# Optimization experiments

Hardware: AMD Instinct MI355X
Metric: run time of the kernel (lower is better)

## Reference

```python
import math
import jax, jax.numpy as jnp
import numpy as np

H = 768      # hidden_size
NH = 12      # num_attention_heads
K = 3        # attention_num branches (wid = None, 2, 4)
DIV = 5.0    # gauss_divisor = 2**(attention_num-1) + 1
SFT = 1.0    # sft_factor
WIDTHS = (None, 2.0, 4.0)
B, L = 4, 1024


def _layernorm(x, s, b, eps=1e-5):
    m = jnp.mean(x, axis=-1, keepdims=True)
    v = jnp.mean((x - m) ** 2, axis=-1, keepdims=True)
    return (x - m) / jnp.sqrt(v + eps) * s + b


def _log_gauss_bias(props_len, width):
    # matches generate_gauss_weight + log(clamp_min(1e-6))
    center = jnp.arange(props_len, dtype=jnp.float32) / props_len          # (L,)
    wt = jnp.maximum(jnp.float32(width), 0.01) / DIV                       # scalar
    pos = jnp.linspace(0.0, 1.0, props_len)                                # (L,)
    g = (0.3989422804014327 / wt) * jnp.exp(-(pos[None, :] - center[:, None]) ** 2 / (2.0 * wt * wt))
    g = g / jnp.max(g, axis=-1, keepdims=True)
    return jnp.log(jnp.maximum(g, 1e-6))                                   # (L, L)


def _attn(qx, kx, vx, Wq, bq, Wk, bk, Wv, bv, bias, mask):
    Bn, Lq, D = qx.shape
    dh = D // NH
    q = (qx @ Wq + bq).reshape(Bn, Lq, NH, dh)
    k = (kx @ Wk + bk).reshape(Bn, kx.shape[1], NH, dh)
    v = (vx @ Wv + bv).reshape(Bn, vx.shape[1], NH, dh)
    s = jnp.einsum('bqhd,bkhd->bhqk', q, k) / math.sqrt(dh)
    if bias is not None:
        s = s + bias[None, None]                  # cached Gaussian log-bias
    if mask is not None:
        s = s + (1.0 - mask)[:, None, None, :] * (-10000.0)
    p = jax.nn.softmax(s, axis=-1)
    return jnp.einsum('bhqk,bkhd->bqhd', p, v).reshape(Bn, Lq, D)


def _block(x, mask, Wq, bq, Wk, bk, Wv, bv, W1, b1, W2, b2, n1s, n1b, n2s, n2b, bias):
    a = _attn(x, x, x, Wq, bq, Wk, bk, Wv, bv, bias, mask)
    x = _layernorm(x + a, n1s, n1b)
    h = jax.nn.relu(x @ W1 + b1) @ W2 + b2
    return _layernorm(x + h, n2s, n2b)


def setup_inputs():
    key = jax.random.key(0)
    ks = iter(jax.random.split(key, 64))
    def p(*sh):
        return jax.random.normal(next(ks), sh, dtype=jnp.float32) * 0.02
    inp = {}
    inp['input_tensor'] = jax.random.normal(next(ks), (B, L, H), dtype=jnp.float32)
    inp['attention_mask'] = jnp.ones((B, L), dtype=jnp.float32)
    for nm, sh in [('bWq', (K, H, H)), ('bWk', (K, H, H)), ('bWv', (K, H, H)),
                   ('bW1', (K, H, 4 * H)), ('bW2', (K, 4 * H, H)),
                   ('caWq', (H, H)), ('caWk', (H, H)), ('caWv', (H, H)),
                   ('caW1', (H, H)), ('caW2', (H, H)), ('Wl1', (H, H)), ('Wl2', (H, 1))]:
        inp[nm] = p(*sh)
    for nm, sh in [('bbq', (K, H)), ('bbk', (K, H)), ('bbv', (K, H)), ('bb1', (K, 4 * H)), ('bb2', (K, H)),
                   ('cabq', (H,)), ('cabk', (H,)), ('cabv', (H,)), ('cab1', (H,)), ('cab2', (H,)),
                   ('bl1', (H,)), ('bl2', (1,))]:
        inp[nm] = jnp.zeros(sh, dtype=jnp.float32)
    for nm, sh in [('bn1s', (K, H)), ('bn2s', (K, H)), ('bns', (H,)), ('can1s', (H,)), ('can2s', (H,))]:
        inp[nm] = jnp.ones(sh, dtype=jnp.float32)
    for nm, sh in [('bn1b', (K, H)), ('bn2b', (K, H)), ('bnb', (H,)), ('can1b', (H,)), ('can2b', (H,))]:
        inp[nm] = jnp.zeros(sh, dtype=jnp.float32)
    return inp


def reference(input_tensor, attention_mask, bWq, bbq, bWk, bbk, bWv, bbv, bW1, bb1, bW2, bb2,
              bn1s, bn1b, bn2s, bn2b, bns, bnb,
              caWq, cabq, caWk, cabk, caWv, cabv, caW1, cab1, caW2, cab2,
              can1s, can1b, can2s, can2b, Wl1, bl1, Wl2, bl2):
    Bn, Ln, _ = input_tensor.shape
    mask = attention_mask
    biases = [None if w is None else _log_gauss_bias(Ln, w) for w in WIDTHS]
    outs = []
    for i in range(K):
        o = _block(input_tensor, mask,
                   bWq[i], bbq[i], bWk[i], bbk[i], bWv[i], bbv[i],
                   bW1[i], bb1[i], bW2[i], bb2[i],
                   bn1s[i], bn1b[i], bn2s[i], bn2b[i], biases[i])
        outs.append(_layernorm(o, bns, bnb))
    oo = jnp.stack(outs, axis=-1)                                   # (B, L, H, K)
    valid = mask                                                    # (B, L)
    denom = jnp.maximum(valid.sum(axis=1, keepdims=True), 1.0)      # (B, 1)
    mean_token = (oo.mean(-1) * valid[:, :, None]).sum(axis=1, keepdims=True) / denom[:, :, None]  # (B,1,H)
    selected = mean_token  # weight_token=None, mode='global' -> global_token = mean_token
    branch_feat = jnp.transpose(oo, (0, 3, 1, 2)).reshape(Bn * K, Ln, H)
    query_token = jnp.repeat(selected, K, axis=0)                   # (B*K, 1, H)
    branch_mask = jnp.repeat(mask, K, axis=0)                       # (B*K, L)
    # CrossAttention (wid=None, FFN d_ff = H)
    a = _attn(query_token, branch_feat, branch_feat, caWq, cabq, caWk, cabk, caWv, cabv, None, branch_mask)
    q = _layernorm(query_token + a, can1s, can1b)
    t = jax.nn.relu(q @ caW1 + cab1) @ caW2 + cab2
    q = _layernorm(q + t, can2s, can2b)                             # (B*K, 1, H)
    w = q.reshape(Bn, K, H)
    w = jax.nn.relu(w @ Wl1 + bl1)
    w = (w @ Wl2 + bl2)[..., 0]                                     # (B, K)
    w = jax.nn.softmax(w / SFT, axis=-1)
    return (oo * w[:, None, None, :]).sum(axis=-1)                  # (B, L, H)
```

## Files before the change

### kernel.cpp

```cpp
#include <hip/hip_runtime.h>
#include <hip/hip_bf16.h>
#include <cstdint>
#include <cmath>

typedef __hip_bfloat16 bf16;
typedef __attribute__((ext_vector_type(8))) __bf16 bf16x8;
typedef __attribute__((ext_vector_type(4))) float f32x4;

#define NE2C ((size_t)4096 * 768)

__device__ inline float ldv(const void* __restrict__ p, size_t i, bool b){
  return b ? __bfloat162float(((const bf16*)p)[i]) : ((const float*)p)[i];
}

__device__ inline float wave_sum(float v){
  #pragma unroll
  for (int o = 1; o < 64; o <<= 1) v += __shfl_xor(v, o, 64);
  return v;
}
__device__ inline float wave_max(float v){
  #pragma unroll
  for (int o = 1; o < 64; o <<= 1) v = fmaxf(v, __shfl_xor(v, o, 64));
  return v;
}

__device__ __forceinline__ void gload_lds16(const __bf16* g, __bf16* l){
  __builtin_amdgcn_global_load_lds(
      (const __attribute__((address_space(1))) uint32_t*)g,
      (__attribute__((address_space(3))) uint32_t*)l,
      16, 0, 0);
}

__global__ void flag_kernel(const void* __restrict__ bns, int* __restrict__ flagp){
  if (threadIdx.x == 0) flagp[0] = (((const uint32_t*)bns)[0] == 0x3F800000u) ? 0 : 1;
}

__global__ __launch_bounds__(256) void maskchk_kernel(const void* __restrict__ mask, int* __restrict__ flagp){
  const bool isb = flagp[0] != 0;
  int t = threadIdx.x;
  int ok = 1;
  for (int j = t; j < 4096; j += 256) ok &= (ldv(mask, (size_t)j, isb) == 1.0f) ? 1 : 0;
  __shared__ int allok;
  if (t == 0) allok = 1;
  __syncthreads();
  if (!ok) atomicAnd(&allok, 0);
  __syncthreads();
  if (t == 0) flagp[1] = allok;
}

__global__ __launch_bounds__(256) void cvtb_kernel(const void* __restrict__ in, __bf16* __restrict__ out,
                                                   int n, const int* __restrict__ flagp){
  const bool isb = flagp[0] != 0;
  int i = blockIdx.x * 256 + threadIdx.x;
  if (i < n) out[i] = (__bf16)ldv(in, i, isb);
}

__global__ __launch_bounds__(256) void transpose_kernel(const void* __restrict__ in, size_t in_off, size_t in_zstride,
    __bf16* __restrict__ out, size_t out_off, size_t out_zstride, int K, int N, const int* __restrict__ flagp)
{
  const bool isb = flagp[0] != 0;
  const int z = blockIdx.z;
  const size_t ioff = in_off + (size_t)z * in_zstride;
  __bf16* op = out + out_off + (size_t)z * out_zstride;
  const int n0 = blockIdx.x * 64, k0 = blockIdx.y * 64;
  __shared__ __bf16 T[64][65];
  const int cr = threadIdx.x >> 6, cc = threadIdx.x & 63;
  #pragma unroll
  for (int it = 0; it < 16; ++it) {
    int r = it * 4 + cr;
    T[r][cc] = (__bf16)ldv(in, ioff + (size_t)(k0 + r) * N + (n0 + cc), isb);
  }
  __syncthreads();
  #pragma unroll
  for (int it = 0; it < 16; ++it) {
    int r = it * 4 + cr;
    op[(size_t)(n0 + r) * K + (k0 + cc)] = T[cc][r];
  }
}

__global__ __launch_bounds__(256) void biaspack_kernel(const void* bbq, const void* bbk, const void* bbv,
    const void* bb1, const void* bb2, const void* cabk, const void* cabv,
    float* __restrict__ pool, const int* __restrict__ flagp)
{
  const bool isb = flagp[0] != 0;
  int idx = blockIdx.x * 256 + threadIdx.x;
  if (idx >= 19968) return;
  float v;
  if (idx < 6912) {
    int i = idx / 2304, rem = idx % 2304;
    int m = rem / 768, c = rem % 768;
    const void* src = (m == 0) ? bbq : ((m == 1) ? bbk : bbv);
    v = ldv(src, (size_t)i * 768 + c, isb);
  } else if (idx < 16128) v = ldv(bb1, idx - 6912, isb);
  else if (idx < 18432)   v = ldv(bb2, idx - 16128, isb);
  else if (idx < 19200)   v = ldv(cabk, idx - 18432, isb);
  else                    v = ldv(cabv, idx - 19200, isb);
  pool[idx] = v;
}

__global__ __launch_bounds__(256) void gaussbias_kernel(float* __restrict__ gb)
{
  const int br = blockIdx.x >> 10;
  const int q  = blockIdx.x & 1023;
  const float inv2wt2 = (br == 0) ? 3.125f : 0.78125f;
  const float c2 = inv2wt2 * 1.4426950408889634f;
  const float cq = (float)q * (1.f / 1024.f);
  const float kst = roundf(cq * 1023.f);
  const float dd = kst * (1.f / 1023.f) - cq;
  const float dmin = dd * dd;
  float* row = gb + (size_t)br * 1048576 + (size_t)q * 1024;
  for (int o = threadIdx.x; o < 1024; o += 256) {
    int cb = o >> 6, rem = o & 63, rr = rem >> 2, t = rem & 3;
    int k = cb * 64 + t * 16 + rr;
    float d2 = (float)k * (1.f / 1023.f) - cq;
    row[o] = fmaxf((dmin - d2 * d2) * c2, -19.9315686f);
  }
}

__global__ __launch_bounds__(256) void gemm_mfma_kernel(
    const __bf16* __restrict__ A, size_t a_zstride,
    const __bf16* __restrict__ WT, const float* __restrict__ biasp,
    __bf16* __restrict__ C, int M, int N, int K, int relu)
{
  const int z = blockIdx.z;
  A  += (size_t)z * a_zstride;
  WT += (size_t)z * (size_t)N * K;
  biasp += (size_t)z * N;
  C  += (size_t)z * (size_t)M * N;
  const int m0 = blockIdx.y * 128, n0 = blockIdx.x * 128;
  const int tid = threadIdx.x, w = tid >> 6, lane = tid & 63;
  const int quad = lane >> 4, r16 = lane & 15;
  const int wr = w >> 1, wc = w & 1;
  __shared__ __align__(16) __bf16 As[128 * 32];
  __shared__ __align__(16) __bf16 Bs[128 * 32];
  f32x4 acc[4][4];
  #pragma unroll
  for (int i = 0; i < 4; ++i)
    #pragma unroll
    for (int j = 0; j < 4; ++j) acc[i][j] = (f32x4){0.f, 0.f, 0.f, 0.f};

  const int srow = tid >> 2;
  const int scc  = (tid & 3) * 8;

  for (int k0 = 0; k0 < K; k0 += 32) {
    __syncthreads();
    #pragma unroll
    for (int it = 0; it < 2; ++it) {
      int row = it * 64 + srow;
      const __bf16* gA = A  + (size_t)(m0 + row) * K + k0 + scc;
      const __bf16* gB = WT + (size_t)(n0 + row) * K + k0 + scc;
      __bf16* lA = &As[(it * 256 + w * 64) * 8];
      __bf16* lB = &Bs[(it * 256 + w * 64) * 8];
      gload_lds16(gA, lA);
      gload_lds16(gB, lB);
    }
    __syncthreads();
    bf16x8 af[4], bf[4];
    #pragma unroll
    for (int mt = 0; mt < 4; ++mt) af[mt] = *(const bf16x8*)&As[(wr * 64 + mt * 16 + r16) * 32 + quad * 8];
    #pragma unroll
    for (int nt = 0; nt < 4; ++nt) bf[nt] = *(const bf16x8*)&Bs[(wc * 64 + nt * 16 + r16) * 32 + quad * 8];
    #pragma unroll
    for (int mt = 0; mt < 4; ++mt)
      #pragma unroll
      for (int nt = 0; nt < 4; ++nt)
        acc[mt][nt] = __builtin_amdgcn_mfma_f32_16x16x32_bf16(af[mt], bf[nt], acc[mt][nt], 0, 0, 0);
  }
  #pragma unroll
  for (int nt = 0; nt < 4; ++nt) {
    int col = n0 + wc * 64 + nt * 16 + r16;
    float bv = biasp[col];
    #pragma unroll
    for (int mt = 0; mt < 4; ++mt) {
      int rowb = m0 + wr * 64 + mt * 16 + quad * 4;
      #pragma unroll
      for (int reg = 0; reg < 4; ++reg) {
        float v = acc[mt][nt][reg] + bv;
        if (relu) v = fmaxf(v, 0.f);
        C[(size_t)(rowb + reg) * N + col] = (__bf16)v;
      }
    }
  }
}

__global__ __launch_bounds__(256) void gemm_small_kernel(const float* __restrict__ A, const void* __restrict__ W,
    size_t woff, const void* __restrict__ bias, size_t boff, float* __restrict__ C,
    int N, int K, int relu, const int* __restrict__ flagp)
{
  const bool isb = flagp[0] != 0;
  const int row = blockIdx.y;
  const int c = blockIdx.x * 64 + (threadIdx.x & 63);
  const int ks = threadIdx.x >> 6;
  const int klen = K >> 2;
  const float* ar = A + (size_t)row * K + ks * klen;
  const size_t wbase = woff + (size_t)ks * klen * N + c;
  float acc = 0.f;
  #pragma unroll 4
  for (int k = 0; k < klen; ++k)
    acc += ar[k] * ldv(W, wbase + (size_t)k * N, isb);
  __shared__ float red[4][64];
  red[ks][threadIdx.x & 63] = acc;
  __syncthreads();
  if (threadIdx.x < 64) {
    float v = red[0][threadIdx.x] + red[1][threadIdx.x] + red[2][threadIdx.x] + red[3][threadIdx.x];
    v += ldv(bias, boff + c, isb);
    if (relu) v = fmaxf(v, 0.f);
    C[(size_t)row * N + c] = v;
  }
}

__global__ __launch_bounds__(256) void attn_mfma_kernel(
    const __bf16* __restrict__ QKV, const void* __restrict__ mask,
    const float* __restrict__ gbias,
    __bf16* __restrict__ Aout, const int* __restrict__ flagp)
{
  const bool isb = flagp[0] != 0;
  const bool mall = flagp[1] != 0;
  const int bz = blockIdx.z;
  const int b = bz & 3, br = bz >> 2;
  const __bf16* Q  = QKV + (size_t)br * 3 * NE2C;
  const __bf16* Kg = Q + NE2C;
  const __bf16* Vg = Q + 2 * NE2C;
  Aout += (size_t)br * NE2C;
  const int has_bias = br > 0;

  const int h = blockIdx.y;
  const int tid = threadIdx.x;
  const int w = tid >> 6, lane = tid & 63;
  const int quad = lane >> 4, r16 = lane & 15;
  const int qbase = blockIdx.x * 64 + w * 16;

  __shared__ __align__(16) __bf16 Ks[64 * 72];
  __shared__ __align__(16) __bf16 Vt[64 * 72];
  __shared__ __align__(16) __bf16 Ps[4][16 * 72];

  const __bf16* qrow = Q + ((size_t)(b * 1024 + qbase + r16)) * 768 + h * 64;
  bf16x8 aq0 = *(const bf16x8*)(qrow + quad * 8);
  bf16x8 aq1 = *(const bf16x8*)(qrow + 32 + quad * 8);

  const float* bq4[4];
  if (has_bias) {
    const float* gbb = gbias + (size_t)(br - 1) * 1048576 + r16 * 4;
    #pragma unroll
    for (int reg = 0; reg < 4; ++reg)
      bq4[reg] = gbb + (size_t)(qbase + quad * 4 + reg) * 1024;
  }

  float m_r[4], l_r[4];
  f32x4 O[4];
  #pragma unroll
  for (int n = 0; n < 4; ++n) O[n] = (f32x4){0.f, 0.f, 0.f, 0.f};
  #pragma unroll
  for (int reg = 0; reg < 4; ++reg) { m_r[reg] = -1e30f; l_r[reg] = 0.f; }

  const int dd = tid & 63;
  const int rb = tid >> 6;
  const int dswz = (dd >> 3) & 7;

  const int kr_row0 = tid >> 3;
  const int kr_c8   = (tid & 7) * 8;
  const size_t kcol  = (size_t)h * 64 + kr_c8;
  const size_t vcol  = (size_t)h * 64 + dd;
  const size_t bbase = (size_t)b * 1024;

  const float SCL = 0.18033688f;
  const float MBIG = 14426.9504f;
  const float THR2 = 11.5415603f;

  bf16x8 kpre0, kpre1;
  bf16x8 vpre0, vpre1;

  {
    kpre0 = *(const bf16x8*)(Kg + (bbase + kr_row0)      * 768 + kcol);
    kpre1 = *(const bf16x8*)(Kg + (bbase + kr_row0 + 32) * 768 + kcol);
    const int r0 = rb * 16;
    #pragma unroll
    for (int i = 0; i < 8; ++i) {
      vpre0[i] = Vg[(bbase + r0 + i)     * 768 + vcol];
      vpre1[i] = Vg[(bbase + r0 + 8 + i) * 768 + vcol];
    }
  }

  for (int c0 = 0; c0 < 1024; c0 += 64) {
    __syncthreads();
    *(bf16x8*)&Ks[kr_row0 * 72 + kr_c8]        = kpre0;
    *(bf16x8*)&Ks[(kr_row0 + 32) * 72 + kr_c8] = kpre1;
    {
      int blk0 = ((rb * 16)     >> 3) ^ dswz;
      int blk1 = ((rb * 16 + 8) >> 3) ^ dswz;
      *(bf16x8*)&Vt[dd * 72 + blk0 * 8] = vpre0;
      *(bf16x8*)&Vt[dd * 72 + blk1 * 8] = vpre1;
    }
    __syncthreads();

    if (c0 + 64 < 1024) {
      const size_t cb = bbase + c0 + 64;
      kpre0 = *(const bf16x8*)(Kg + (cb + kr_row0)      * 768 + kcol);
      kpre1 = *(const bf16x8*)(Kg + (cb + kr_row0 + 32) * 768 + kcol);
      const int r0 = rb * 16;
      #pragma unroll
      for (int i = 0; i < 8; ++i) {
        vpre0[i] = Vg[(cb + r0 + i)     * 768 + vcol];
        vpre1[i] = Vg[(cb + r0 + 8 + i) * 768 + vcol];
      }
    }

    f32x4 bv4[4];
    if (has_bias) {
      #pragma unroll
      for (int reg = 0; reg < 4; ++reg) bv4[reg] = *(const f32x4*)(bq4[reg] + c0);
    }

    float s4[4][4], p4[4][4];
    #pragma unroll
    for (int t = 0; t < 4; ++t) {
      bf16x8 b0 = *(const bf16x8*)&Ks[(t * 16 + r16) * 72 + quad * 8];
      bf16x8 b1 = *(const bf16x8*)&Ks[(t * 16 + r16) * 72 + 32 + quad * 8];
      f32x4 accq = (f32x4){0.f, 0.f, 0.f, 0.f};
      accq = __builtin_amdgcn_mfma_f32_16x16x32_bf16(aq0, b0, accq, 0, 0, 0);
      accq = __builtin_amdgcn_mfma_f32_16x16x32_bf16(aq1, b1, accq, 0, 0, 0);
      float mterm = 0.f;
      if (!mall) {
        int kk = c0 + t * 16 + r16;
        float mk = ldv(mask, (size_t)(b * 1024 + kk), isb);
        mterm = fmaf(mk, MBIG, -MBIG);
      }
      if (has_bias) {
        #pragma unroll
        for (int reg = 0; reg < 4; ++reg)
          s4[t][reg] = fmaf(accq[reg], SCL, mterm) + bv4[reg][t];
      } else {
        #pragma unroll
        for (int reg = 0; reg < 4; ++reg)
          s4[t][reg] = fmaf(accq[reg], SCL, mterm);
      }
    }
    float mlane[4];
    #pragma unroll
    for (int reg = 0; reg < 4; ++reg)
      mlane[reg] = fmaxf(fmaxf(s4[0][reg], s4[1][reg]), fmaxf(s4[2][reg], s4[3][reg]));
    bool need = (mlane[0] > m_r[0] + THR2) || (mlane[1] > m_r[1] + THR2)
             || (mlane[2] > m_r[2] + THR2) || (mlane[3] > m_r[3] + THR2);
    if (__any(need)) {
      #pragma unroll
      for (int reg = 0; reg < 4; ++reg) {
        float t0 = mlane[reg];
        #pragma unroll
        for (int off = 1; off < 16; off <<= 1) t0 = fmaxf(t0, __shfl_xor(t0, off, 64));
        float mnew = fmaxf(m_r[reg], t0);
        float alpha = exp2f(m_r[reg] - mnew);
        l_r[reg] *= alpha;
        m_r[reg] = mnew;
        #pragma unroll
        for (int n = 0; n < 4; ++n) O[n][reg] *= alpha;
      }
    }
    #pragma unroll
    for (int reg = 0; reg < 4; ++reg) {
      float rs = 0.f;
      #pragma unroll
      for (int t = 0; t < 4; ++t) { float p = exp2f(s4[t][reg] - m_r[reg]); p4[t][reg] = p; rs += p; }
      l_r[reg] += rs;
    }
    __bf16* pw = &Ps[w][0];
    #pragma unroll
    for (int t = 0; t < 4; ++t)
      #pragma unroll
      for (int reg = 0; reg < 4; ++reg)
        pw[(quad * 4 + reg) * 72 + t * 16 + r16] = (__bf16)p4[t][reg];
    bf16x8 ap0 = *(const bf16x8*)&pw[r16 * 72 + quad * 8];
    bf16x8 ap1 = *(const bf16x8*)&pw[r16 * 72 + 32 + quad * 8];
    __builtin_amdgcn_s_setprio(1);
    #pragma unroll
    for (int n = 0; n < 4; ++n) {
      int dr = n * 16 + r16;
      int sw = (dr >> 3) & 7;
      bf16x8 bv0 = *(const bf16x8*)&Vt[dr * 72 + (quad ^ sw) * 8];
      bf16x8 bv1 = *(const bf16x8*)&Vt[dr * 72 + ((quad + 4) ^ sw) * 8];
      O[n] = __builtin_amdgcn_mfma_f32_16x16x32_bf16(ap0, bv0, O[n], 0, 0, 0);
      O[n] = __builtin_amdgcn_mfma_f32_16x16x32_bf16(ap1, bv1, O[n], 0, 0, 0);
    }
    __builtin_amdgcn_s_setprio(0);
  }
  #pragma unroll
  for (int reg = 0; reg < 4; ++reg) {
    float lv = l_r[reg];
    #pragma unroll
    for (int off = 1; off < 16; off <<= 1) lv += __shfl_xor(lv, off, 64);
    l_r[reg] = lv;
  }
  #pragma unroll
  for (int n = 0; n < 4; ++n)
    #pragma unroll
    for (int reg = 0; reg < 4; ++reg) {
      int qg = qbase + quad * 4 + reg;
      Aout[((size_t)(b * 1024 + qg)) * 768 + h * 64 + n * 16 + r16] = (__bf16)(O[n][reg] / l_r[reg]);
    }
}

__global__ __launch_bounds__(256) void lnb_b_kernel(const __bf16* __restrict__ x, const __bf16* __restrict__ a,
    const void* __restrict__ sc, const void* __restrict__ bi, __bf16* __restrict__ out,
    const int* __restrict__ flagp)
{
  const bool isb = flagp[0] != 0;
  const int br = blockIdx.y;
  a   += (size_t)br * NE2C;
  out += (size_t)br * NE2C;
  const size_t so = (size_t)br * 768;
  int r = blockIdx.x;
  const __bf16* xr = x + (size_t)r * 768;
  const __bf16* ar = a + (size_t)r * 768;
  int t = threadIdx.x;
  float v[3]; float s = 0.f, ss = 0.f;
  #pragma unroll
  for (int j = 0; j < 3; j++) {
    int c = t + j * 256;
    float val = (float)xr[c] + (float)ar[c];
    v[j] = val; s += val; ss += val * val;
  }
  s = wave_sum(s); ss = wave_sum(ss);
  __shared__ float sred[8];
  __shared__ float stats[2];
  int lane = t & 63, wid = t >> 6;
  if (lane == 0) { sred[wid] = s; sred[4 + wid] = ss; }
  __syncthreads();
  if (t == 0) {
    float S = sred[0] + sred[1] + sred[2] + sred[3];
    float SS = sred[4] + sred[5] + sred[6] + sred[7];
    float mean = S * (1.f / 768.f);
    float var = fmaxf(SS * (1.f / 768.f) - mean * mean, 0.f);
    stats[0] = mean; stats[1] = rsqrtf(var + 1e-5f);
  }
  __syncthreads();
  float mean = stats[0], rstd = stats[1];
  #pragma unroll
  for (int j = 0; j < 3; j++) {
    int c = t + j * 256;
    out[(size_t)r * 768 + c] = (__bf16)((v[j] - mean) * rstd * ldv(sc, so + c, isb) + ldv(bi, so + c, isb));
  }
}

__global__ __launch_bounds__(256) void lnb2_b_kernel(const __bf16* __restrict__ x, const __bf16* __restrict__ a,
    const void* __restrict__ sc1, const void* __restrict__ bi1,
    const void* __restrict__ sc2, const void* __restrict__ bi2,
    __bf16* __restrict__ out, const int* __restrict__ flagp)
{
  const bool isb = flagp[0] != 0;
  const int br = blockIdx.y;
  x   += (size_t)br * NE2C;
  a   += (size_t)br * NE2C;
  out += (size_t)br * NE2C;
  const size_t s1off = (size_t)br * 768;
  int r = blockIdx.x;
  const __bf16* xr = x + (size_t)r * 768;
  const __bf16* ar = a + (size_t)r * 768;
  int t = threadIdx.x;
  int lane = t & 63, wid = t >> 6;
  __shared__ float sred[8], stats[2], sred2[8], stats2[2];

  float v[3]; float s = 0.f, ss = 0.f;
  #pragma unroll
  for (int j = 0; j < 3; j++) {
    int c = t + j * 256;
    float val = (float)xr[c] + (float)ar[c];
    v[j] = val; s += val; ss += val * val;
  }
  s = wave_sum(s); ss = wave_sum(ss);
  if (lane == 0) { sred[wid] = s; sred[4 + wid] = ss; }
  __syncthreads();
  if (t == 0) {
    float S = sred[0] + sred[1] + sred[2] + sred[3];
    float SS = sred[4] + sred[5] + sred[6] + sred[7];
    float mean = S * (1.f / 768.f);
    float var = fmaxf(SS * (1.f / 768.f) - mean * mean, 0.f);
    stats[0] = mean; stats[1] = rsqrtf(var + 1e-5f);
  }
  __syncthreads();
  float mean = stats[0], rstd = stats[1];
  float y[3]; float s2 = 0.f, ss2 = 0.f;
  #pragma unroll
  for (int j = 0; j < 3; j++) {
    int c = t + j * 256;
    float yv = (v[j] - mean) * rstd * ldv(sc1, s1off + c, isb) + ldv(bi1, s1off + c, isb);
    yv = (float)(__bf16)yv;
    y[j] = yv; s2 += yv; ss2 += yv * yv;
  }
  s2 = wave_sum(s2); ss2 = wave_sum(ss2);
  if (lane == 0) { sred2[wid] = s2; sred2[4 + wid] = ss2; }
  __syncthreads();
  if (t == 0) {
    float S = sred2[0] + sred2[1] + sred2[2] + sred2[3];
    float SS = sred2[4] + sred2[5] + sred2[6] + sred2[7];
    float mean2 = S * (1.f / 768.f);
    float var2 = fmaxf(SS * (1.f / 768.f) - mean2 * mean2, 0.f);
    stats2[0] = mean2; stats2[1] = rsqrtf(var2 + 1e-5f);
  }
  __syncthreads();
  float mean2 = stats2[0], rstd2 = stats2[1];
  #pragma unroll
  for (int j = 0; j < 3; j++) {
    int c = t + j * 256;
    out[(size_t)r * 768 + c] = (__bf16)((y[j] - mean2) * rstd2 * ldv(sc2, c, isb) + ldv(bi2, c, isb));
  }
}

__global__ __launch_bounds__(256) void ln_kernel(const float* __restrict__ x, const float* __restrict__ a,
    const void* __restrict__ sc, size_t soff, const void* __restrict__ bi, size_t boff,
    float* __restrict__ out, int xdiv, const int* __restrict__ flagp)
{
  const bool isb = flagp[0] != 0;
  int r = blockIdx.x;
  const float* xr = x + (size_t)(xdiv > 1 ? r / xdiv : r) * 768;
  const float* ar = a ? a + (size_t)r * 768 : nullptr;
  int t = threadIdx.x;
  float v[3]; float s = 0.f, ss = 0.f;
  #pragma unroll
  for (int j = 0; j < 3; j++) {
    int c = t + j * 256;
    float val = xr[c] + (ar ? ar[c] : 0.f);
    v[j] = val; s += val; ss += val * val;
  }
  s = wave_sum(s); ss = wave_sum(ss);
  __shared__ float sred[8];
  __shared__ float stats[2];
  int lane = t & 63, wid = t >> 6;
  if (lane == 0) { sred[wid] = s; sred[4 + wid] = ss; }
  __syncthreads();
  if (t == 0) {
    float S = sred[0] + sred[1] + sred[2] + sred[3];
    float SS = sred[4] + sred[5] + sred[6] + sred[7];
    float mean = S * (1.f / 768.f);
    float var = fmaxf(SS * (1.f / 768.f) - mean * mean, 0.f);
    stats[0] = mean; stats[1] = rsqrtf(var + 1e-5f);
  }
  __syncthreads();
  float mean = stats[0], rstd = stats[1];
  #pragma unroll
  for (int j = 0; j < 3; j++) {
    int c = t + j * 256;
    out[(size_t)r * 768 + c] = (v[j] - mean) * rstd * ldv(sc, soff + c, isb) + ldv(bi, boff + c, isb);
  }
}

__global__ __launch_bounds__(256) void meantok_part_kernel(const __bf16* __restrict__ OO, const void* __restrict__ mask,
    float* __restrict__ partials, const int* __restrict__ flagp)
{
  const bool isb = flagp[0] != 0;
  const size_t NE = NE2C;
  int h = blockIdx.x * 256 + threadIdx.x;
  int b = blockIdx.y, lc = blockIdx.z;
  const __bf16* base = OO + (size_t)(b * 1024 + lc * 64) * 768 + h;
  float acc = 0.f;
  for (int l = 0; l < 64; ++l) {
    float mk = ldv(mask, (size_t)(b * 1024 + lc * 64 + l), isb);
    size_t off = (size_t)l * 768;
    acc += mk * ((float)base[off] + (float)base[off + NE] + (float)base[off + 2 * NE]);
  }
  partials[((size_t)(b * 16 + lc)) * 768 + h] = acc;
}

__global__ __launch_bounds__(256) void meantok_fin_kernel(const float* __restrict__ partials,
    const void* __restrict__ mask, float* __restrict__ mt, const int* __restrict__ flagp)
{
  const bool isb = flagp[0] != 0;
  int h = blockIdx.x * 256 + threadIdx.x;
  int b = blockIdx.y;
  int t = threadIdx.x;
  float ms = 0.f;
  for (int j = t; j < 1024; j += 256) ms += ldv(mask, (size_t)(b * 1024 + j), isb);
  ms = wave_sum(ms);
  __shared__ float sred[4];
  __shared__ float msume;
  if ((t & 63) == 0) sred[t >> 6] = ms;
  __syncthreads();
  if (t == 0) msume = fmaxf(sred[0] + sred[1] + sred[2] + sred[3], 1.f);
  __syncthreads();
  float acc = 0.f;
  #pragma unroll
  for (int lc = 0; lc < 16; ++lc) acc += partials[((size_t)(b * 16 + lc)) * 768 + h];
  mt[b * 768 + h] = acc * (1.f / 3.f) / msume;
}

__global__ __launch_bounds__(256) void crossattn_kernel(const float* __restrict__ qC, const __bf16* __restrict__ kC,
    const __bf16* __restrict__ vC, const void* __restrict__ mask, float* __restrict__ caout,
    const int* __restrict__ flagp)
{
  const bool isb = flagp[0] != 0;
  const bool mall = flagp[1] != 0;
  int h = blockIdx.x, i = blockIdx.y, b = blockIdx.z;
  int tid = threadIdx.x, lane = tid & 63, wv = tid >> 6;
  __shared__ float sbuf[1024];
  __shared__ float qsh[64];
  __shared__ float red[8];
  __shared__ float vred[4][64];
  if (tid < 64) qsh[tid] = qC[b * 768 + h * 64 + tid];
  __syncthreads();
  const size_t rowbase = (size_t)(i * 4 + b) * 1024;
  const __bf16* kb = kC + rowbase * 768 + h * 64;
  float lmax = -1e30f;
  for (int j = tid; j < 1024; j += 256) {
    const __bf16* kr = kb + (size_t)j * 768;
    float s = 0.f;
    #pragma unroll
    for (int d0 = 0; d0 < 8; ++d0) {
      bf16x8 kv = *(const bf16x8*)(kr + d0 * 8);
      #pragma unroll
      for (int e = 0; e < 8; ++e) s += qsh[d0 * 8 + e] * (float)kv[e];
    }
    s *= 0.125f;
    if (!mall) {
      float mk = ldv(mask, (size_t)(b * 1024 + j), isb);
      s += (1.0f - mk) * (-10000.0f);
    }
    sbuf[j] = s;
    lmax = fmaxf(lmax, s);
  }
  lmax = wave_max(lmax);
  if (lane == 0) red[wv] = lmax;
  __syncthreads();
  float mm = fmaxf(fmaxf(red[0], red[1]), fmaxf(red[2], red[3]));
  float lsum = 0.f;
  for (int j = tid; j < 1024; j += 256) {
    float p = __expf(sbuf[j] - mm);
    sbuf[j] = p;
    lsum += p;
  }
  lsum = wave_sum(lsum);
  if (lane == 0) red[4 + wv] = lsum;
  __syncthreads();
  float L = red[4] + red[5] + red[6] + red[7];
  const __bf16* vb = vC + rowbase * 768 + h * 64;
  float acc = 0.f;
  for (int j = wv * 256; j < wv * 256 + 256; ++j)
    acc += sbuf[j] * (float)vb[(size_t)j * 768 + lane];
  vred[wv][lane] = acc;
  __syncthreads();
  if (tid < 64) {
    float a = vred[0][tid] + vred[1][tid] + vred[2][tid] + vred[3][tid];
    caout[(size_t)(b * 3 + i) * 768 + h * 64 + tid] = a / L;
  }
}

__global__ __launch_bounds__(256) void logits_kernel(const float* __restrict__ wfeat, const void* __restrict__ Wl2,
    const void* __restrict__ bl2, float* __restrict__ logits, const int* __restrict__ flagp)
{
  const bool isb = flagp[0] != 0;
  int r = blockIdx.x, t = threadIdx.x;
  float s = 0.f;
  #pragma unroll
  for (int j = 0; j < 3; j++) {
    int c = t + j * 256;
    s += wfeat[(size_t)r * 768 + c] * ldv(Wl2, c, isb);
  }
  s = wave_sum(s);
  __shared__ float sred[4];
  if ((t & 63) == 0) sred[t >> 6] = s;
  __syncthreads();
  if (t == 0) logits[r] = sred[0] + sred[1] + sred[2] + sred[3] + ldv(bl2, 0, isb);
}

__global__ void wsoftmax_kernel(const float* __restrict__ logits, float* __restrict__ w)
{
  int b = threadIdx.x;
  if (b < 4) {
    float l0 = logits[b * 3], l1 = logits[b * 3 + 1], l2 = logits[b * 3 + 2];
    float m = fmaxf(l0, fmaxf(l1, l2));
    float e0 = __expf(l0 - m), e1 = __expf(l1 - m), e2 = __expf(l2 - m);
    float inv = 1.f / (e0 + e1 + e2);
    w[b * 3] = e0 * inv; w[b * 3 + 1] = e1 * inv; w[b * 3 + 2] = e2 * inv;
  }
}

__global__ __launch_bounds__(256) void combine_kernel(const __bf16* __restrict__ OO, const float* __restrict__ w,
                                                      void* __restrict__ out, const int* __restrict__ flagp)
{
  const bool isb = flagp[0] != 0;
  const size_t NE = NE2C;
  size_t idx = (size_t)blockIdx.x * 256 + threadIdx.x;
  int b = (int)(idx / (1024 * 768));
  float w0 = w[b * 3], w1 = w[b * 3 + 1], w2 = w[b * 3 + 2];
  float v = (float)OO[idx] * w0 + (float)OO[idx + NE] * w1 + (float)OO[idx + 2 * NE] * w2;
  if (isb) ((bf16*)out)[idx] = __float2bfloat16(v);
  else     ((float*)out)[idx] = v;
}

extern "C" void kernel_launch(void* const* d_in, const int* in_sizes, int n_in,
                              void* d_out, int out_size, void* d_ws, size_t ws_size,
                              hipStream_t stream)
{
  const void* X    = d_in[0];
  const void* mask = d_in[1];
  const void* bWq  = d_in[2];
  const void* bWk  = d_in[3];
  const void* bWv  = d_in[4];
  const void* bW1  = d_in[5];
  const void* bW2  = d_in[6];
  const void* caWq = d_in[7];
  const void* caWk = d_in[8];
  const void* caWv = d_in[9];
  const void* caW1 = d_in[10];
  const void* caW2 = d_in[11];
  const void* Wl1  = d_in[12];
  const void* Wl2  = d_in[13];
  const void* bbq  = d_in[14];
  const void* bbk  = d_in[15];
  const void* bbv  = d_in[16];
  const void* bb1  = d_in[17];
  const void* bb2  = d_in[18];
  const void* cabq = d_in[19];
  const void* cabk = d_in[20];
  const void* cabv = d_in[21];
  const void* cab1 = d_in[22];
  const void* cab2 = d_in[23];
  const void* bl1  = d_in[24];
  const void* bl2  = d_in[25];
  const void* bn1s = d_in[26];
  const void* bn2s = d_in[27];
  const void* bns  = d_in[28];
  const void* can1s= d_in[29];
  const void* can2s= d_in[30];
  const void* bn1b = d_in[31];
  const void* bn2b = d_in[32];
  const void* bnb  = d_in[33];
  const void* can1b= d_in[34];
  const void* can2b= d_in[35];

  const size_t NE2 = NE2C;
  const size_t WSQ = (size_t)768 * 768;
  const size_t WSF = (size_t)768 * 3072;

  __bf16* XFb  = (__bf16*)d_ws;
  __bf16* Rb   = XFb + NE2;
  __bf16* X1   = Rb + 12 * NE2;
  __bf16* AF2  = X1 + 3 * NE2;
  __bf16* WTqkv= AF2 + 3 * NE2;
  __bf16* WT1  = WTqkv + 9 * WSQ;
  __bf16* WT2  = WT1 + 3 * WSF;
  __bf16* WTc  = WT2 + 3 * WSF;
  float*  pool = (float*)(WTc + 2 * WSQ);
  float*  mt     = pool + 19968;
  float*  qC     = mt + 3072;
  float*  caout  = qC + 3072;
  float*  q1     = caout + 9216;
  float*  t1     = q1 + 9216;
  float*  t2     = t1 + 9216;
  float*  q2     = t2 + 9216;
  float*  wfeat  = q2 + 9216;
  float*  logits = wfeat + 9216;
  float*  wsm    = logits + 16;
  int*    flagp  = (int*)(wsm + 16);
  float*  partials = (float*)(flagp + 64);
  __bf16* OO = X1;
  __bf16* kC = Rb;
  __bf16* vC = Rb + 3 * NE2;
  float*  gb = (float*)X1;

  dim3 blk256(256);
  flag_kernel<<<dim3(1), dim3(64), 0, stream>>>(bns, flagp);
  maskchk_kernel<<<dim3(1), blk256, 0, stream>>>(mask, flagp);
  cvtb_kernel<<<dim3((int)((NE2 + 255) / 256)), blk256, 0, stream>>>(X, XFb, (int)NE2, flagp);

  transpose_kernel<<<dim3(12, 12, 3), blk256, 0, stream>>>(bWq, 0, WSQ, WTqkv, 0 * WSQ, 3 * WSQ, 768, 768, flagp);
  transpose_kernel<<<dim3(12, 12, 3), blk256, 0, stream>>>(bWk, 0, WSQ, WTqkv, 1 * WSQ, 3 * WSQ, 768, 768, flagp);
  transpose_kernel<<<dim3(12, 12, 3), blk256, 0, stream>>>(bWv, 0, WSQ, WTqkv, 2 * WSQ, 3 * WSQ, 768, 768, flagp);
  transpose_kernel<<<dim3(48, 12, 3), blk256, 0, stream>>>(bW1, 0, WSF, WT1, 0, WSF, 768, 3072, flagp);
  transpose_kernel<<<dim3(12, 48, 3), blk256, 0, stream>>>(bW2, 0, WSF, WT2, 0, WSF, 3072, 768, flagp);
  transpose_kernel<<<dim3(12, 12, 1), blk256, 0, stream>>>(caWk, 0, 0, WTc, 0, 0, 768, 768, flagp);
  transpose_kernel<<<dim3(12, 12, 1), blk256, 0, stream>>>(caWv, 0, 0, WTc, WSQ, 0, 768, 768, flagp);
  biaspack_kernel<<<dim3(78), blk256, 0, stream>>>(bbq, bbk, bbv, bb1, bb2, cabk, cabv, pool, flagp);
  gaussbias_kernel<<<dim3(2048), blk256, 0, stream>>>(gb);

  gemm_mfma_kernel<<<dim3(6, 32, 9), blk256, 0, stream>>>(XFb, 0, WTqkv, pool, Rb, 4096, 768, 768, 0);
  attn_mfma_kernel<<<dim3(16, 12, 12), blk256, 0, stream>>>(Rb, mask, gb, AF2, flagp);
  lnb_b_kernel<<<dim3(4096, 3), blk256, 0, stream>>>(XFb, AF2, bn1s, bn1b, X1, flagp);
  gemm_mfma_kernel<<<dim3(24, 32, 3), blk256, 0, stream>>>(X1, NE2, WT1, pool + 6912, Rb, 4096, 3072, 768, 1);
  gemm_mfma_kernel<<<dim3(6, 32, 3), blk256, 0, stream>>>(Rb, 4 * NE2, WT2, pool + 16128, AF2, 4096, 768, 3072, 0);
  lnb2_b_kernel<<<dim3(4096, 3), blk256, 0, stream>>>(X1, AF2, bn2s, bn2b, bns, bnb, OO, flagp);

  meantok_part_kernel<<<dim3(3, 4, 16), blk256, 0, stream>>>(OO, mask, partials, flagp);
  meantok_fin_kernel<<<dim3(3, 4), blk256, 0, stream>>>(partials, mask, mt, flagp);
  gemm_small_kernel<<<dim3(12, 4), blk256, 0, stream>>>(mt, caWq, 0, cabq, 0, qC, 768, 768, 0, flagp);
  gemm_mfma_kernel<<<dim3(6, 96, 2), blk256, 0, stream>>>(OO, 0, WTc, pool + 18432, kC, 12288, 768, 768, 0);
  crossattn_kernel<<<dim3(12, 3, 4), blk256, 0, stream>>>(qC, kC, vC, mask, caout, flagp);
  ln_kernel<<<dim3(12), blk256, 0, stream>>>(mt, caout, can1s, 0, can1b, 0, q1, 3, flagp);
  gemm_small_kernel<<<dim3(12, 12), blk256, 0, stream>>>(q1, caW1, 0, cab1, 0, t1, 768, 768, 1, flagp);
  gemm_small_kernel<<<dim3(12, 12), blk256, 0, stream>>>(t1, caW2, 0, cab2, 0, t2, 768, 768, 0, flagp);
  ln_kernel<<<dim3(12), blk256, 0, stream>>>(q1, t2, can2s, 0, can2b, 0, q2, 1, flagp);
  gemm_small_kernel<<<dim3(12, 12), blk256, 0, stream>>>(q2, Wl1, 0, bl1, 0, wfeat, 768, 768, 1, flagp);
  logits_kernel<<<dim3(12), blk256, 0, stream>>>(wfeat, Wl2, bl2, logits, flagp);
  wsoftmax_kernel<<<dim3(1), dim3(64), 0, stream>>>(logits, wsm);
  combine_kernel<<<dim3((int)(NE2 / 256)), blk256, 0, stream>>>(OO, wsm, d_out, flagp);
}
```

Baseline: 933.9 us.

## Write V transposed from QKV GEMM so attention loads V tiles with vector reads

The QKV projection GEMM now stores the V output in a per-batch transposed (feature-major, token-contiguous) layout. The attention kernel can then fetch V tiles with 16-byte vector loads instead of 16 scalar strided loads per thread, and writes them into the swizzled LDS tile directly. The cost moves to the GEMM epilogue, whose transposed stores are strided and poorly coalesced, and that may offset the savings in attention.

```diff
diff --git a/kernel.cpp b/kernel.cpp
--- a/kernel.cpp
+++ b/kernel.cpp
@@ -120,13 +120,14 @@
 __global__ __launch_bounds__(256) void gemm_mfma_kernel(
     const __bf16* __restrict__ A, size_t a_zstride,
     const __bf16* __restrict__ WT, const float* __restrict__ biasp,
-    __bf16* __restrict__ C, int M, int N, int K, int relu)
+    __bf16* __restrict__ C, int M, int N, int K, int relu, int tmode)
 {
   const int z = blockIdx.z;
   A  += (size_t)z * a_zstride;
   WT += (size_t)z * (size_t)N * K;
   biasp += (size_t)z * N;
   C  += (size_t)z * (size_t)M * N;
+  const bool tvout = (tmode != 0) && (z % 3 == 2);
   const int m0 = blockIdx.y * 128, n0 = blockIdx.x * 128;
   const int tid = threadIdx.x, w = tid >> 6, lane = tid & 63;
   const int quad = lane >> 4, r16 = lane & 15;
@@ -177,7 +178,12 @@
       for (int reg = 0; reg < 4; ++reg) {
         float v = acc[mt][nt][reg] + bv;
         if (relu) v = fmaxf(v, 0.f);
-        C[(size_t)(rowb + reg) * N + col] = (__bf16)v;
+        if (tvout) {
+          int row = rowb + reg;
+          C[(size_t)(row >> 10) * 786432 + (size_t)col * 1024 + (row & 1023)] = (__bf16)v;
+        } else {
+          C[(size_t)(rowb + reg) * N + col] = (__bf16)v;
+        }
       }
     }
   }
@@ -220,7 +226,7 @@
   const int b = bz & 3, br = bz >> 2;
   const __bf16* Q  = QKV + (size_t)br * 3 * NE2C;
   const __bf16* Kg = Q + NE2C;
-  const __bf16* Vg = Q + 2 * NE2C;
+  const __bf16* VgT = Q + 2 * NE2C + (size_t)b * 786432;
   Aout += (size_t)br * NE2C;
   const int has_bias = br > 0;
 
@@ -253,56 +259,40 @@
   #pragma unroll
   for (int reg = 0; reg < 4; ++reg) { m_r[reg] = -1e30f; l_r[reg] = 0.f; }
 
-  const int dd = tid & 63;
-  const int rb = tid >> 6;
-  const int dswz = (dd >> 3) & 7;
-
-  const int kr_row0 = tid >> 3;
-  const int kr_c8   = (tid & 7) * 8;
-  const size_t kcol  = (size_t)h * 64 + kr_c8;
-  const size_t vcol  = (size_t)h * 64 + dd;
+  const int sr0  = tid >> 3;
+  const int sc8  = (tid & 7) * 8;
+  const size_t kcol  = (size_t)h * 64 + sc8;
   const size_t bbase = (size_t)b * 1024;
+  const __bf16* vbase0 = VgT + (size_t)(h * 64 + sr0)      * 1024 + sc8;
+  const __bf16* vbase1 = VgT + (size_t)(h * 64 + sr0 + 32) * 1024 + sc8;
+  const int vls0 = sr0 * 72        + (((sc8 >> 3) ^ ((sr0 >> 3) & 7)) * 8);
+  const int vls1 = (sr0 + 32) * 72 + (((sc8 >> 3) ^ (((sr0 + 32) >> 3) & 7)) * 8);
 
   const float SCL = 0.18033688f;
   const float MBIG = 14426.9504f;
   const float THR2 = 11.5415603f;
 
-  bf16x8 kpre0, kpre1;
-  bf16x8 vpre0, vpre1;
-
-  {
-    kpre0 = *(const bf16x8*)(Kg + (bbase + kr_row0)      * 768 + kcol);
-    kpre1 = *(const bf16x8*)(Kg + (bbase + kr_row0 + 32) * 768 + kcol);
-    const int r0 = rb * 16;
-    #pragma unroll
-    for (int i = 0; i < 8; ++i) {
-      vpre0[i] = Vg[(bbase + r0 + i)     * 768 + vcol];
-      vpre1[i] = Vg[(bbase + r0 + 8 + i) * 768 + vcol];
-    }
-  }
+  bf16x8 kpre0, kpre1, vpre0, vpre1;
+
+  kpre0 = *(const bf16x8*)(Kg + (bbase + sr0)      * 768 + kcol);
+  kpre1 = *(const bf16x8*)(Kg + (bbase + sr0 + 32) * 768 + kcol);
+  vpre0 = *(const bf16x8*)(vbase0);
+  vpre1 = *(const bf16x8*)(vbase1);
 
   for (int c0 = 0; c0 < 1024; c0 += 64) {
     __syncthreads();
-    *(bf16x8*)&Ks[kr_row0 * 72 + kr_c8]        = kpre0;
-    *(bf16x8*)&Ks[(kr_row0 + 32) * 72 + kr_c8] = kpre1;
-    {
-      int blk0 = ((rb * 16)     >> 3) ^ dswz;
-      int blk1 = ((rb * 16 + 8) >> 3) ^ dswz;
-      *(bf16x8*)&Vt[dd * 72 + blk0 * 8] = vpre0;
-      *(bf16x8*)&Vt[dd * 72 + blk1 * 8] = vpre1;
-    }
+    *(bf16x8*)&Ks[sr0 * 72 + sc8]        = kpre0;
+    *(bf16x8*)&Ks[(sr0 + 32) * 72 + sc8] = kpre1;
+    *(bf16x8*)&Vt[vls0] = vpre0;
+    *(bf16x8*)&Vt[vls1] = vpre1;
     __syncthreads();
 
     if (c0 + 64 < 1024) {
       const size_t cb = bbase + c0 + 64;
-      kpre0 = *(const bf16x8*)(Kg + (cb + kr_row0)      * 768 + kcol);
-      kpre1 = *(const bf16x8*)(Kg + (cb + kr_row0 + 32) * 768 + kcol);
-      const int r0 = rb * 16;
-      #pragma unroll
-      for (int i = 0; i < 8; ++i) {
-        vpre0[i] = Vg[(cb + r0 + i)     * 768 + vcol];
-        vpre1[i] = Vg[(cb + r0 + 8 + i) * 768 + vcol];
-      }
+      kpre0 = *(const bf16x8*)(Kg + (cb + sr0)      * 768 + kcol);
+      kpre1 = *(const bf16x8*)(Kg + (cb + sr0 + 32) * 768 + kcol);
+      vpre0 = *(const bf16x8*)(vbase0 + c0 + 64);
+      vpre1 = *(const bf16x8*)(vbase1 + c0 + 64);
     }
 
     f32x4 bv4[4];
@@ -770,17 +760,17 @@
   biaspack_kernel<<<dim3(78), blk256, 0, stream>>>(bbq, bbk, bbv, bb1, bb2, cabk, cabv, pool, flagp);
   gaussbias_kernel<<<dim3(2048), blk256, 0, stream>>>(gb);
 
-  gemm_mfma_kernel<<<dim3(6, 32, 9), blk256, 0, stream>>>(XFb, 0, WTqkv, pool, Rb, 4096, 768, 768, 0);
+  gemm_mfma_kernel<<<dim3(6, 32, 9), blk256, 0, stream>>>(XFb, 0, WTqkv, pool, Rb, 4096, 768, 768, 0, 1);
   attn_mfma_kernel<<<dim3(16, 12, 12), blk256, 0, stream>>>(Rb, mask, gb, AF2, flagp);
   lnb_b_kernel<<<dim3(4096, 3), blk256, 0, stream>>>(XFb, AF2, bn1s, bn1b, X1, flagp);
-  gemm_mfma_kernel<<<dim3(24, 32, 3), blk256, 0, stream>>>(X1, NE2, WT1, pool + 6912, Rb, 4096, 3072, 768, 1);
-  gemm_mfma_kernel<<<dim3(6, 32, 3), blk256, 0, stream>>>(Rb, 4 * NE2, WT2, pool + 16128, AF2, 4096, 768, 3072, 0);
+  gemm_mfma_kernel<<<dim3(24, 32, 3), blk256, 0, stream>>>(X1, NE2, WT1, pool + 6912, Rb, 4096, 3072, 768, 1, 0);
+  gemm_mfma_kernel<<<dim3(6, 32, 3), blk256, 0, stream>>>(Rb, 4 * NE2, WT2, pool + 16128, AF2, 4096, 768, 3072, 0, 0);
   lnb2_b_kernel<<<dim3(4096, 3), blk256, 0, stream>>>(X1, AF2, bn2s, bn2b, bns, bnb, OO, flagp);
 
   meantok_part_kernel<<<dim3(3, 4, 16), blk256, 0, stream>>>(OO, mask, partials, flagp);
   meantok_fin_kernel<<<dim3(3, 4), blk256, 0, stream>>>(partials, mask, mt, flagp);
   gemm_small_kernel<<<dim3(12, 4), blk256, 0, stream>>>(mt, caWq, 0, cabq, 0, qC, 768, 768, 0, flagp);
-  gemm_mfma_kernel<<<dim3(6, 96, 2), blk256, 0, stream>>>(OO, 0, WTc, pool + 18432, kC, 12288, 768, 768, 0);
+  gemm_mfma_kernel<<<dim3(6, 96, 2), blk256, 0, stream>>>(OO, 0, WTc, pool + 18432, kC, 12288, 768, 768, 0, 0);
   crossattn_kernel<<<dim3(12, 3, 4), blk256, 0, stream>>>(qC, kC, vC, mask, caout, flagp);
   ln_kernel<<<dim3(12), blk256, 0, stream>>>(mt, caout, can1s, 0, can1b, 0, q1, 3, flagp);
   gemm_small_kernel<<<dim3(12, 12), blk256, 0, stream>>>(q1, caW1, 0, cab1, 0, t1, 768, 768, 1, flagp);
```

Measured after the change: 967.5 us. 3.6% more time.

## Pre-transpose V globally and double attention block query tile to 128

Applied to the files above, without the earlier changes.

A new kernel writes V transposed per batch and branch into scratch space after the QKV GEMM. The attention kernel then loads V^T with vectorized 16-byte loads in place of strided scalar gathers. The attention block also grows to 512 threads covering 128 queries, so each K/V tile staged in shared memory is reused by eight waves instead of four. The cost is an extra global read and write of V plus a launch, and each K/V tile is now loaded in one pass per thread.

```diff
diff --git a/kernel.cpp b/kernel.cpp
--- a/kernel.cpp
+++ b/kernel.cpp
@@ -75,6 +75,28 @@
   for (int it = 0; it < 16; ++it) {
     int r = it * 4 + cr;
     op[(size_t)(n0 + r) * K + (k0 + cc)] = T[cc][r];
+  }
+}
+
+__global__ __launch_bounds__(256) void vtrans_kernel(const __bf16* __restrict__ Rb, __bf16* __restrict__ VT)
+{
+  const int z = blockIdx.z;
+  const int br = z >> 2, b = z & 3;
+  const __bf16* src = Rb + (size_t)(br * 3 + 2) * NE2C;
+  __bf16* dst = VT + (size_t)z * 786432;
+  const int c0 = blockIdx.x * 64, k0 = blockIdx.y * 64;
+  __shared__ __bf16 T[64][65];
+  const int cr = threadIdx.x >> 6, cc = threadIdx.x & 63;
+  #pragma unroll
+  for (int it = 0; it < 16; ++it) {
+    int k = it * 4 + cr;
+    T[k][cc] = src[((size_t)(b * 1024 + k0 + k)) * 768 + c0 + cc];
+  }
+  __syncthreads();
+  #pragma unroll
+  for (int it = 0; it < 16; ++it) {
+    int c = it * 4 + cr;
+    dst[(size_t)(c0 + c) * 1024 + k0 + cc] = T[cc][c];
   }
 }
 
@@ -209,7 +231,7 @@
   }
 }
 
-__global__ __launch_bounds__(256) void attn_mfma_kernel(
+__global__ __launch_bounds__(512) void attn_mfma_kernel(
     const __bf16* __restrict__ QKV, const void* __restrict__ mask,
     const float* __restrict__ gbias,
     __bf16* __restrict__ Aout, const int* __restrict__ flagp)
@@ -220,7 +242,7 @@
   const int b = bz & 3, br = bz >> 2;
   const __bf16* Q  = QKV + (size_t)br * 3 * NE2C;
   const __bf16* Kg = Q + NE2C;
-  const __bf16* Vg = Q + 2 * NE2C;
+  const __bf16* VgT = QKV + 9 * NE2C + (size_t)bz * 786432;
   Aout += (size_t)br * NE2C;
   const int has_bias = br > 0;
 
@@ -228,11 +250,11 @@
   const int tid = threadIdx.x;
   const int w = tid >> 6, lane = tid & 63;
   const int quad = lane >> 4, r16 = lane & 15;
-  const int qbase = blockIdx.x * 64 + w * 16;
+  const int qbase = blockIdx.x * 128 + w * 16;
 
   __shared__ __align__(16) __bf16 Ks[64 * 72];
   __shared__ __align__(16) __bf16 Vt[64 * 72];
-  __shared__ __align__(16) __bf16 Ps[4][16 * 72];
+  __shared__ __align__(16) __bf16 Ps[8][16 * 72];
 
   const __bf16* qrow = Q + ((size_t)(b * 1024 + qbase + r16)) * 768 + h * 64;
   bf16x8 aq0 = *(const bf16x8*)(qrow + quad * 8);
@@ -253,56 +275,30 @@
   #pragma unroll
   for (int reg = 0; reg < 4; ++reg) { m_r[reg] = -1e30f; l_r[reg] = 0.f; }
 
-  const int dd = tid & 63;
-  const int rb = tid >> 6;
-  const int dswz = (dd >> 3) & 7;
-
-  const int kr_row0 = tid >> 3;
-  const int kr_c8   = (tid & 7) * 8;
-  const size_t kcol  = (size_t)h * 64 + kr_c8;
-  const size_t vcol  = (size_t)h * 64 + dd;
+  const int sr0  = tid >> 3;
+  const int sc8  = (tid & 7) * 8;
+  const size_t kcol  = (size_t)h * 64 + sc8;
   const size_t bbase = (size_t)b * 1024;
+  const __bf16* vbase = VgT + (size_t)(h * 64 + sr0) * 1024 + sc8;
+  const int vls = sr0 * 72 + (((sc8 >> 3) ^ ((sr0 >> 3) & 7)) * 8);
 
   const float SCL = 0.18033688f;
   const float MBIG = 14426.9504f;
   const float THR2 = 11.5415603f;
 
-  bf16x8 kpre0, kpre1;
-  bf16x8 vpre0, vpre1;
-
-  {
-    kpre0 = *(const bf16x8*)(Kg + (bbase + kr_row0)      * 768 + kcol);
-    kpre1 = *(const bf16x8*)(Kg + (bbase + kr_row0 + 32) * 768 + kcol);
-    const int r0 = rb * 16;
-    #pragma unroll
-    for (int i = 0; i < 8; ++i) {
-      vpre0[i] = Vg[(bbase + r0 + i)     * 768 + vcol];
-      vpre1[i] = Vg[(bbase + r0 + 8 + i) * 768 + vcol];
-    }
-  }
+  bf16x8 kpre, vpre;
+  kpre = *(const bf16x8*)(Kg + (bbase + sr0) * 768 + kcol);
+  vpre = *(const bf16x8*)(vbase);
 
   for (int c0 = 0; c0 < 1024; c0 += 64) {
     __syncthreads();
-    *(bf16x8*)&Ks[kr_row0 * 72 + kr_c8]        = kpre0;
-    *(bf16x8*)&Ks[(kr_row0 + 32) * 72 + kr_c8] = kpre1;
-    {
-      int blk0 = ((rb * 16)     >> 3) ^ dswz;
-      int blk1 = ((rb * 16 + 8) >> 3) ^ dswz;
-      *(bf16x8*)&Vt[dd * 72 + blk0 * 8] = vpre0;
-      *(bf16x8*)&Vt[dd * 72 + blk1 * 8] = vpre1;
-    }
+    *(bf16x8*)&Ks[sr0 * 72 + sc8] = kpre;
+    *(bf16x8*)&Vt[vls] = vpre;
     __syncthreads();
 
     if (c0 + 64 < 1024) {
-      const size_t cb = bbase + c0 + 64;
-      kpre0 = *(const bf16x8*)(Kg + (cb + kr_row0)      * 768 + kcol);
-      kpre1 = *(const bf16x8*)(Kg + (cb + kr_row0 + 32) * 768 + kcol);
-      const int r0 = rb * 16;
-      #pragma unroll
-      for (int i = 0; i < 8; ++i) {
-        vpre0[i] = Vg[(cb + r0 + i)     * 768 + vcol];
-        vpre1[i] = Vg[(cb + r0 + 8 + i) * 768 + vcol];
-      }
+      kpre = *(const bf16x8*)(Kg + (bbase + c0 + 64 + sr0) * 768 + kcol);
+      vpre = *(const bf16x8*)(vbase + c0 + 64);
     }
 
     f32x4 bv4[4];
@@ -753,6 +749,7 @@
   __bf16* OO = X1;
   __bf16* kC = Rb;
   __bf16* vC = Rb + 3 * NE2;
+  __bf16* VT = Rb + 9 * NE2;
   float*  gb = (float*)X1;
 
   dim3 blk256(256);
@@ -771,7 +768,8 @@
   gaussbias_kernel<<<dim3(2048), blk256, 0, stream>>>(gb);
 
   gemm_mfma_kernel<<<dim3(6, 32, 9), blk256, 0, stream>>>(XFb, 0, WTqkv, pool, Rb, 4096, 768, 768, 0);
-  attn_mfma_kernel<<<dim3(16, 12, 12), blk256, 0, stream>>>(Rb, mask, gb, AF2, flagp);
+  vtrans_kernel<<<dim3(12, 16, 12), blk256, 0, stream>>>(Rb, VT);
+  attn_mfma_kernel<<<dim3(8, 12, 12), dim3(512), 0, stream>>>(Rb, mask, gb, AF2, flagp);
   lnb_b_kernel<<<dim3(4096, 3), blk256, 0, stream>>>(XFb, AF2, bn1s, bn1b, X1, flagp);
   gemm_mfma_kernel<<<dim3(24, 32, 3), blk256, 0, stream>>>(X1, NE2, WT1, pool + 6912, Rb, 4096, 3072, 768, 1);
   gemm_mfma_kernel<<<dim3(6, 32, 3), blk256, 0, stream>>>(Rb, 4 * NE2, WT2, pool + 16128, AF2, 4096, 768, 3072, 0);
```

New measurement: 924.0 us. Within noise of the previous version (-1.1%).
